# Kernel tuning notes

Hardware: AMD Instinct MI355X
Metric: run time of the kernel (lower is better)

## Reference

```python
import jax, jax.numpy as jnp
import numpy as np

NUM_ITER = 3  # Newton-Schulz iterations (init kwarg)

def setup_inputs() -> dict:
    key = jax.random.key(0)
    x = jax.random.normal(key, (64, 28, 28, 256), dtype=jnp.float32)
    return {"x": x}

def reference(x):
    B, H, W, C = x.shape
    n = H * W
    # Faithful to K.reshape(inputs, (batch, C, n)) -- a plain row-major reshape
    X = x.reshape(B, C, n)
    # Sigma = X @ I_hat @ X^T with I_hat = (1/n)(I - (1/n) 11^T), i.e. the
    # centering projector: identical to mean-centering then (1/n) Xc Xc^T.
    Xc = X - X.mean(axis=2, keepdims=True)            # [B, C, n]
    Sigma = jnp.einsum('bcn,bdn->bcd', Xc, Xc) / n    # [B, C, C]
    trace = jnp.trace(Sigma, axis1=1, axis2=2)[:, None, None]  # [B,1,1]
    A = Sigma / trace
    I = jnp.eye(C, dtype=x.dtype)
    I3 = 3.0 * I
    Y = A
    Z = jnp.broadcast_to(I, (B, C, C))
    # Newton-Schulz: NOTE original updates Z with the already-updated Y
    for _ in range(NUM_ITER):
        Y = 0.5 * jnp.matmul(Y, I3 - jnp.matmul(Z, Y))
        Z = 0.5 * jnp.matmul(I3 - jnp.matmul(Z, Y), Z)
    Cmat = jnp.sqrt(trace) * Y                        # [B, C, C]
    # Upper-triangular (incl. diagonal) vectorization, row-major order
    iu_r, iu_c = jnp.triu_indices(C)
    return Cmat[:, iu_r, iu_c]                        # [B, C*(C+1)/2]
```

## Files before the change

### kernel.cpp

```cpp
#include <hip/hip_runtime.h>
#include <math.h>

#define BATCH 64
#define CD 256
#define NX 784
#define TRIU_N 32896
#define MSZ 65536
#define REG_STRIDE 1032
#define ARR_STRIDE 4128
#define BUF_STRIDE 16512

typedef unsigned short ushort_t;
typedef unsigned int uint_t;
typedef __attribute__((ext_vector_type(8))) short short8;
typedef __attribute__((ext_vector_type(16))) float floatx16;

__device__ __forceinline__ void decode_bid(int bid, int& tile, int& bb) {
    int xcd = bid & 7, g = bid >> 3;
    tile = g & 3;
    bb = ((g >> 2) << 3) | xcd;
}

__device__ __forceinline__ float bf2f(ushort_t h) {
    return __uint_as_float(((uint_t)h) << 16);
}
__device__ __forceinline__ void pack2(float f0, float f1, uint_t& hp, uint_t& lp) {
    uint_t h, l;
    asm("v_cvt_pk_bf16_f32 %0, %1, %2" : "=v"(h) : "v"(f0), "v"(f1));
    float r0 = f0 - __uint_as_float(h << 16);
    float r1 = f1 - __uint_as_float(h & 0xffff0000u);
    asm("v_cvt_pk_bf16_f32 %0, %1, %2" : "=v"(l) : "v"(r0), "v"(r1));
    hp = h; lp = l;
}
__device__ __forceinline__ void store8(ushort_t* H, ushort_t* L, const float* y) {
    uint_t hw[4], lw[4];
    #pragma unroll
    for (int i = 0; i < 4; ++i) pack2(y[2*i], y[2*i+1], hw[i], lw[i]);
    *(uint4*)H = make_uint4(hw[0], hw[1], hw[2], hw[3]);
    *(uint4*)L = make_uint4(lw[0], lw[1], lw[2], lw[3]);
}

__device__ __forceinline__ int swoff(int r, int c) {
    int p = r >> 7, s = (c >> 5) & 7, ks = (c >> 4) & 1, kh = (c >> 3) & 1;
    return ((((p * 8 + s) * 2 + ks) * 2 + kh) * 128 + (r & 127)) * 8 + (c & 7);
}

__device__ __forceinline__ void rawbar() {
    __builtin_amdgcn_s_barrier();
    __builtin_amdgcn_sched_barrier(0);
}

__device__ __forceinline__ void mfma_stage8(const ushort_t* us, int bufbase,
                                            int wr, int wcp, int khalf, int lrow,
                                            floatx16* acc) {
    __builtin_amdgcn_s_setprio(1);
    #pragma unroll
    for (int ks = 0; ks < 2; ++ks) {
        const int rid = ks * 2 + khalf;
        const ushort_t* rb = us + bufbase + rid * REG_STRIDE + lrow * 8;
        short8 aH = *(const short8*)(rb + wr * 256);
        short8 aL = *(const short8*)(rb + ARR_STRIDE + wr * 256);
        #pragma unroll
        for (int cq = 0; cq < 2; ++cq) {
            const int col = wcp * 2 + cq;
            short8 bH = *(const short8*)(rb + 2 * ARR_STRIDE + col * 256);
            short8 bL = *(const short8*)(rb + 3 * ARR_STRIDE + col * 256);
            acc[cq] = __builtin_amdgcn_mfma_f32_32x32x16_bf16(aH, bH, acc[cq], 0, 0, 0);
            acc[cq] = __builtin_amdgcn_mfma_f32_32x32x16_bf16(aH, bL, acc[cq], 0, 0, 0);
            acc[cq] = __builtin_amdgcn_mfma_f32_32x32x16_bf16(aL, bH, acc[cq], 0, 0, 0);
        }
    }
    __builtin_amdgcn_s_setprio(0);
}

__device__ __forceinline__ void acc_bounce(float* fsmem, const floatx16* acc,
                                           int wr, int wcp, int khalf, int lrow) {
    __syncthreads();
    #pragma unroll
    for (int cq = 0; cq < 2; ++cq)
        #pragma unroll
        for (int i = 0; i < 16; ++i) {
            int rl = (i & 3) + ((i >> 2) << 3) + (khalf << 2);
            fsmem[(wr * 32 + rl) * 129 + (wcp * 2 + cq) * 32 + lrow] = acc[cq][i];
        }
    __syncthreads();
}

struct Cur { float4 v[2][2]; };

__device__ __forceinline__ void gr_load(const float* Xb, int rowBase, int colBase, int s,
                                        const int* side, const int* srow, const int* skq,
                                        Cur& c) {
    #pragma unroll
    for (int q = 0; q < 2; ++q) {
        int gk = s * 32 + skq[q] * 8;
        if (gk < NX) {
            const float* p = Xb + (size_t)((side[q] ? colBase : rowBase) + srow[q]) * NX + gk;
            c.v[q][0] = *(const float4*)p;
            c.v[q][1] = *(const float4*)(p + 4);
        } else {
            c.v[q][0] = make_float4(0.f, 0.f, 0.f, 0.f);
            c.v[q][1] = make_float4(0.f, 0.f, 0.f, 0.f);
        }
    }
}

__device__ __forceinline__ void gr_conv(ushort_t* us, int bufbase, const Cur& c,
                                        const int* side, const int* srow, const int* skq,
                                        float* rs) {
    #pragma unroll
    for (int q = 0; q < 2; ++q) {
        float f[8] = {c.v[q][0].x, c.v[q][0].y, c.v[q][0].z, c.v[q][0].w,
                      c.v[q][1].x, c.v[q][1].y, c.v[q][1].z, c.v[q][1].w};
        rs[q] += ((f[0] + f[1]) + (f[2] + f[3])) + ((f[4] + f[5]) + (f[6] + f[7]));
        uint_t hp[4], lp[4];
        #pragma unroll
        for (int i = 0; i < 4; ++i) pack2(f[2*i], f[2*i+1], hp[i], lp[i]);
        int base = bufbase + (side[q] * 2) * ARR_STRIDE + skq[q] * REG_STRIDE + srow[q] * 8;
        *(uint4*)(us + base)              = make_uint4(hp[0], hp[1], hp[2], hp[3]);
        *(uint4*)(us + base + ARR_STRIDE) = make_uint4(lp[0], lp[1], lp[2], lp[3]);
    }
}

__global__ __launch_bounds__(512, 1)
void gram_mfma(const float* __restrict__ X, float* __restrict__ means,
               float* __restrict__ tr,
               ushort_t* __restrict__ Gh, ushort_t* __restrict__ Gl) {
    __shared__ __align__(16) float fsmem[16512];
    __shared__ float dsh[8];
    ushort_t* us = (ushort_t*)fsmem;
    int tile, bb;
    decode_bid(blockIdx.x, tile, bb);
    const int rowBase = (tile >> 1) * 128, colBase = (tile & 1) * 128;
    const int tid = threadIdx.x, lane = tid & 63, wv = tid >> 6;
    const int wr = wv >> 1, wcp = wv & 1;
    const int khalf = lane >> 5, lrow = lane & 31;
    const float* Xb = X + (size_t)bb * CD * NX;

    floatx16 acc[2];
    #pragma unroll
    for (int cq = 0; cq < 2; ++cq)
        #pragma unroll
        for (int i = 0; i < 16; ++i) acc[cq][i] = 0.f;

    int side[2], srow[2], skq[2];
    #pragma unroll
    for (int q = 0; q < 2; ++q) {
        int gid = q * 512 + tid;
        side[q] = gid >> 9;
        srow[q] = (gid >> 2) & 127;
        skq[q]  = gid & 3;
    }
    float rs[2] = {0.f, 0.f};

    Cur curA, curB;
    gr_load(Xb, rowBase, colBase, 0, side, srow, skq, curA);
    gr_load(Xb, rowBase, colBase, 1, side, srow, skq, curB);
    gr_conv(us, 0, curA, side, srow, skq, rs);

    for (int s = 0; s < 25; s += 2) {
        asm volatile("s_waitcnt lgkmcnt(0)" ::: "memory");
        rawbar();
        if (s + 2 <= 24) gr_load(Xb, rowBase, colBase, s + 2, side, srow, skq, curA);
        mfma_stage8(us, 0, wr, wcp, khalf, lrow, acc);
        if (s + 1 <= 24) gr_conv(us, BUF_STRIDE, curB, side, srow, skq, rs);
        if (s + 1 <= 24) {
            asm volatile("s_waitcnt lgkmcnt(0)" ::: "memory");
            rawbar();
            if (s + 3 <= 24) gr_load(Xb, rowBase, colBase, s + 3, side, srow, skq, curB);
            mfma_stage8(us, BUF_STRIDE, wr, wcp, khalf, lrow, acc);
            gr_conv(us, 0, curA, side, srow, skq, rs);
        }
    }

    {
        float r0 = rs[0], r1 = rs[1];
        r0 += __shfl_xor(r0, 1, 64); r0 += __shfl_xor(r0, 2, 64);
        r1 += __shfl_xor(r1, 1, 64); r1 += __shfl_xor(r1, 2, 64);
        if ((tid & 3) == 0) {
            int rr = tid >> 2;
            means[bb * CD + rowBase + rr] = r0 * (1.0f / NX);
            means[bb * CD + colBase + rr] = r1 * (1.0f / NX);
        }
    }

    acc_bounce(fsmem, acc, wr, wcp, khalf, lrow);
    const int rloc = tid & 127;
    const int r = rowBase + rloc;
    const float mr = means[bb * CD + r];
    const bool diagblk = (rowBase == colBase);
    float dv = 0.f;
    #pragma unroll
    for (int gi = 0; gi < 4; ++gi) {
        int g = (tid >> 7) + gi * 4;
        int c0 = colBase + g * 8;
        int so = swoff(r, c0);
        float v[8];
        #pragma unroll
        for (int j = 0; j < 8; ++j) {
            v[j] = fsmem[rloc * 129 + g * 8 + j] * (1.0f / NX) - mr * means[bb * CD + c0 + j];
            if (diagblk && (c0 + j) == r) dv += v[j];
        }
        store8(Gh + (size_t)bb * MSZ + so, Gl + (size_t)bb * MSZ + so, v);
    }
    if (diagblk) {
        for (int off = 32; off; off >>= 1) dv += __shfl_down(dv, off, 64);
        if (lane == 0) dsh[wv] = dv;
        __syncthreads();
        if (tid == 0) {
            float s = ((dsh[0] + dsh[1]) + (dsh[2] + dsh[3]))
                    + ((dsh[4] + dsh[5]) + (dsh[6] + dsh[7]));
            atomicAdd(&tr[bb], s);
        }
    }
}

__device__ __forceinline__ void ns_prefetch(const ushort_t* const* arrp, ushort_t* us,
                                            int wv, int lane, int s, int buf) {
    #pragma unroll
    for (int j = 0; j < 4; ++j) {
        int ck = wv * 4 + j;
        int arr = ck >> 3, rid = (ck >> 1) & 3, half = ck & 1;
        const ushort_t* g = arrp[arr] + s * 4096 + rid * 1024 + half * 512 + lane * 8;
        ushort_t* l = us + buf * BUF_STRIDE + arr * ARR_STRIDE + rid * REG_STRIDE + half * 512;
        __builtin_amdgcn_global_load_lds(
            (const __attribute__((address_space(1))) unsigned int*)g,
            (__attribute__((address_space(3))) unsigned int*)l, 16, 0, 0);
    }
}

template<int MODE>
__global__ __launch_bounds__(512, 1)
void ns_mfma(const ushort_t* __restrict__ Ah, const ushort_t* __restrict__ Al,
             const ushort_t* __restrict__ Bh, const ushort_t* __restrict__ Bl,
             const ushort_t* __restrict__ Mh, const ushort_t* __restrict__ Ml,
             const float* __restrict__ tr,
             ushort_t* __restrict__ O1h, ushort_t* __restrict__ O1l,
             ushort_t* __restrict__ O2h, ushort_t* __restrict__ O2l,
             float* __restrict__ outT) {
    int tile, bb;
    decode_bid(blockIdx.x, tile, bb);
    const int rowBase = (tile >> 1) * 128, colBase = (tile & 1) * 128;
    if (MODE == 3 && rowBase > colBase) return;
    __shared__ __align__(16) float fsmem[33024];
    ushort_t* us = (ushort_t*)fsmem;
    const size_t mb = (size_t)bb * MSZ;
    const int tid = threadIdx.x, lane = tid & 63, wv = tid >> 6;
    const int wr = wv >> 1, wcp = wv & 1;
    const int khalf = lane >> 5, lrow = lane & 31;
    const ushort_t* arrp[4] = {
        Ah + mb + (size_t)(rowBase >> 7) * 32768,
        Al + mb + (size_t)(rowBase >> 7) * 32768,
        Bh + mb + (size_t)(colBase >> 7) * 32768,
        Bl + mb + (size_t)(colBase >> 7) * 32768 };

    floatx16 acc[2];
    #pragma unroll
    for (int cq = 0; cq < 2; ++cq)
        #pragma unroll
        for (int i = 0; i < 16; ++i) acc[cq][i] = 0.f;

    ns_prefetch(arrp, us, wv, lane, 0, 0);
    ns_prefetch(arrp, us, wv, lane, 1, 1);
    ns_prefetch(arrp, us, wv, lane, 2, 2);
    #pragma unroll
    for (int s = 0; s < 8; ++s) {
        if (s <= 5)      asm volatile("s_waitcnt vmcnt(8)" ::: "memory");
        else if (s == 6) asm volatile("s_waitcnt vmcnt(4)" ::: "memory");
        else             asm volatile("s_waitcnt vmcnt(0)" ::: "memory");
        rawbar();
        mfma_stage8(us, (s & 3) * BUF_STRIDE, wr, wcp, khalf, lrow, acc);
        if (s < 5) ns_prefetch(arrp, us, wv, lane, s + 3, (s + 3) & 3);
    }

    acc_bounce(fsmem, acc, wr, wcp, khalf, lrow);
    const int rloc = tid & 127;
    const int r = rowBase + rloc;
    float it = 0.f, st = 0.f;
    if (MODE == 2) it = 1.0f / tr[bb];
    if (MODE == 3) st = sqrtf(tr[bb]);
    #pragma unroll
    for (int gi = 0; gi < 4; ++gi) {
        int g = (tid >> 7) + gi * 4;
        int c0 = colBase + g * 8;
        int so = swoff(r, c0);
        float v[8];
        #pragma unroll
        for (int j = 0; j < 8; ++j) v[j] = fsmem[rloc * 129 + g * 8 + j];
        if (MODE == 0) {
            store8(O1h + mb + so, O1l + mb + so, v);
        } else {
            float mv[8];
            {
                const ushort_t* mhp = Mh + mb + so;
                const ushort_t* mlp = Ml + mb + so;
                uint4 mh4 = *(const uint4*)mhp;
                uint4 ml4 = *(const uint4*)mlp;
                const uint_t mhw[4] = {mh4.x, mh4.y, mh4.z, mh4.w};
                const uint_t mlw[4] = {ml4.x, ml4.y, ml4.z, ml4.w};
                #pragma unroll
                for (int i = 0; i < 4; ++i) {
                    mv[2*i]   = __uint_as_float(mhw[i] << 16) + __uint_as_float(mlw[i] << 16);
                    mv[2*i+1] = __uint_as_float(mhw[i] & 0xffff0000u) + __uint_as_float(mlw[i] & 0xffff0000u);
                }
            }
            if (MODE == 1) {
                float y[8];
                #pragma unroll
                for (int j = 0; j < 8; ++j) y[j] = fmaf(1.5f, mv[j], -0.5f * v[j]);
                store8(O1h + mb + so, O1l + mb + so, y);
            } else if (MODE == 2) {
                float y[8], z[8];
                #pragma unroll
                for (int j = 0; j < 8; ++j) {
                    y[j] = 1.5f * it * mv[j] - 0.5f * it * it * v[j];
                    z[j] = ((r == c0 + j) ? 1.5f : 0.f) - 0.5f * y[j];
                }
                store8(O1h + mb + so, O1l + mb + so, y);
                store8(O2h + mb + so, O2l + mb + so, z);
            } else if (MODE == 4) {
                float w[8];
                #pragma unroll
                for (int j = 0; j < 8; ++j)
                    w[j] = ((r == c0 + j) ? 2.25f : 0.f) - 1.5f * mv[j] + 0.25f * v[j];
                store8(O1h + mb + so, O1l + mb + so, v);
                store8(O2h + mb + so, O2l + mb + so, w);
            } else {
                int tb = r * CD - (r * (r - 1)) / 2 - r;
                #pragma unroll
                for (int j = 0; j < 8; ++j) {
                    float y = fmaf(1.5f, mv[j], -0.5f * v[j]);
                    int c = c0 + j;
                    if (c >= r) outT[(size_t)bb * TRIU_N + tb + c] = st * y;
                }
            }
        }
    }
}

extern "C" void kernel_launch(void* const* d_in, const int* in_sizes, int n_in,
                              void* d_out, int out_size, void* d_ws, size_t ws_size,
                              hipStream_t stream) {
    const float* x = (const float*)d_in[0];
    float* out = (float*)d_out;
    char* ws = (char*)d_ws;
    const size_t HS = (size_t)BATCH * MSZ * 2;
    ushort_t* S0h = (ushort_t*)(ws + 0 * HS);
    ushort_t* S0l = (ushort_t*)(ws + 1 * HS);
    ushort_t* S1h = (ushort_t*)(ws + 2 * HS);
    ushort_t* S1l = (ushort_t*)(ws + 3 * HS);
    ushort_t* S2h = (ushort_t*)(ws + 4 * HS);
    ushort_t* S2l = (ushort_t*)(ws + 5 * HS);
    ushort_t* S3h = (ushort_t*)(ws + 6 * HS);
    ushort_t* S3l = (ushort_t*)(ws + 7 * HS);
    ushort_t* S4h = (ushort_t*)(ws + 8 * HS);
    ushort_t* S4l = (ushort_t*)(ws + 9 * HS);
    float* means = (float*)(ws + 10 * HS);
    float* tr = means + BATCH * CD;

    hipMemsetAsync(tr, 0, BATCH * sizeof(float), stream);
    gram_mfma<<<256, 512, 0, stream>>>(x, means, tr, S0h, S0l);
    ns_mfma<2><<<256, 512, 0, stream>>>(S0h, S0l, S0h, S0l, S0h, S0l, tr,
                                        S1h, S1l, S2h, S2l, nullptr);
    ns_mfma<4><<<256, 512, 0, stream>>>(S1h, S1l, S1h, S1l, S1h, S1l, tr,
                                        S3h, S3l, S0h, S0l, nullptr);
    ns_mfma<1><<<256, 512, 0, stream>>>(S2h, S2l, S3h, S3l, S1h, S1l, tr,
                                        S4h, S4l, nullptr, nullptr, nullptr);
    ns_mfma<1><<<256, 512, 0, stream>>>(S0h, S0l, S4h, S4l, S2h, S2l, tr,
                                        S1h, S1l, nullptr, nullptr, nullptr);
    ns_mfma<0><<<256, 512, 0, stream>>>(S4h, S4l, S4h, S4l, nullptr, nullptr, tr,
                                        S3h, S3l, nullptr, nullptr, nullptr);
    ns_mfma<3><<<256, 512, 0, stream>>>(S1h, S1l, S3h, S3l, S4h, S4l, tr,
                                        nullptr, nullptr, nullptr, nullptr, out);
}
```

Measured before the change: 203.1 us.

## Split output tiles to 128x64 with 256-thread blocks, two per CU

Each block now computes a 128x64 output tile instead of 128x128, so 512 blocks of 256 threads launch per kernel with launch bounds allowing two blocks per CU. The LDS layout is rebuilt with separate A and B regions sized for the narrower B tile. The NS prefetch pipeline drops from four to three stages to fit the smaller shared-memory budget. The aim is better CU occupancy and load balance with 256 CUs, and finer triangular skipping in the final stage, at the cost of reloading A tiles twice as often and a shallower prefetch depth.

```diff
diff --git a/kernel.cpp b/kernel.cpp
--- a/kernel.cpp
+++ b/kernel.cpp
@@ -7,8 +7,11 @@
 #define TRIU_N 32896
 #define MSZ 65536
 #define REG_STRIDE 1032
-#define ARR_STRIDE 4128
-#define BUF_STRIDE 16512
+#define A_ARR 4128
+#define B_BASE 8256
+#define B_REG 520
+#define B_ARR 2080
+#define STG 12416
 
 typedef unsigned short ushort_t;
 typedef unsigned int uint_t;
@@ -17,8 +20,8 @@
 
 __device__ __forceinline__ void decode_bid(int bid, int& tile, int& bb) {
     int xcd = bid & 7, g = bid >> 3;
-    tile = g & 3;
-    bb = ((g >> 2) << 3) | xcd;
+    tile = g & 7;
+    bb = ((g >> 3) << 3) | xcd;
 }
 
 __device__ __forceinline__ float bf2f(ushort_t h) {
@@ -50,21 +53,21 @@
     __builtin_amdgcn_sched_barrier(0);
 }
 
-__device__ __forceinline__ void mfma_stage8(const ushort_t* us, int bufbase,
-                                            int wr, int wcp, int khalf, int lrow,
+__device__ __forceinline__ void mfma_stage4(const ushort_t* us, int bufbase,
+                                            int wv, int khalf, int lrow,
                                             floatx16* acc) {
     __builtin_amdgcn_s_setprio(1);
     #pragma unroll
     for (int ks = 0; ks < 2; ++ks) {
         const int rid = ks * 2 + khalf;
-        const ushort_t* rb = us + bufbase + rid * REG_STRIDE + lrow * 8;
-        short8 aH = *(const short8*)(rb + wr * 256);
-        short8 aL = *(const short8*)(rb + ARR_STRIDE + wr * 256);
+        const ushort_t* ra = us + bufbase + rid * REG_STRIDE + wv * 256 + lrow * 8;
+        short8 aH = *(const short8*)(ra);
+        short8 aL = *(const short8*)(ra + A_ARR);
+        const ushort_t* rb = us + bufbase + B_BASE + rid * B_REG + lrow * 8;
         #pragma unroll
         for (int cq = 0; cq < 2; ++cq) {
-            const int col = wcp * 2 + cq;
-            short8 bH = *(const short8*)(rb + 2 * ARR_STRIDE + col * 256);
-            short8 bL = *(const short8*)(rb + 3 * ARR_STRIDE + col * 256);
+            short8 bH = *(const short8*)(rb + cq * 256);
+            short8 bL = *(const short8*)(rb + B_ARR + cq * 256);
             acc[cq] = __builtin_amdgcn_mfma_f32_32x32x16_bf16(aH, bH, acc[cq], 0, 0, 0);
             acc[cq] = __builtin_amdgcn_mfma_f32_32x32x16_bf16(aH, bL, acc[cq], 0, 0, 0);
             acc[cq] = __builtin_amdgcn_mfma_f32_32x32x16_bf16(aL, bH, acc[cq], 0, 0, 0);
@@ -74,28 +77,29 @@
 }
 
 __device__ __forceinline__ void acc_bounce(float* fsmem, const floatx16* acc,
-                                           int wr, int wcp, int khalf, int lrow) {
+                                           int wv, int khalf, int lrow) {
     __syncthreads();
     #pragma unroll
     for (int cq = 0; cq < 2; ++cq)
         #pragma unroll
         for (int i = 0; i < 16; ++i) {
             int rl = (i & 3) + ((i >> 2) << 3) + (khalf << 2);
-            fsmem[(wr * 32 + rl) * 129 + (wcp * 2 + cq) * 32 + lrow] = acc[cq][i];
+            fsmem[(wv * 32 + rl) * 65 + cq * 32 + lrow] = acc[cq][i];
         }
     __syncthreads();
 }
 
-struct Cur { float4 v[2][2]; };
+struct Cur { float4 v[3][2]; };
 
 __device__ __forceinline__ void gr_load(const float* Xb, int rowBase, int colBase, int s,
-                                        const int* side, const int* srow, const int* skq,
-                                        Cur& c) {
-    #pragma unroll
-    for (int q = 0; q < 2; ++q) {
-        int gk = s * 32 + skq[q] * 8;
+                                        int tid, Cur& c) {
+    const int kq = tid & 3, rr = tid >> 2;
+    const int xrow[3] = {rowBase + rr, rowBase + 64 + rr, colBase + rr};
+    int gk = s * 32 + kq * 8;
+    #pragma unroll
+    for (int q = 0; q < 3; ++q) {
         if (gk < NX) {
-            const float* p = Xb + (size_t)((side[q] ? colBase : rowBase) + srow[q]) * NX + gk;
+            const float* p = Xb + (size_t)xrow[q] * NX + gk;
             c.v[q][0] = *(const float4*)p;
             c.v[q][1] = *(const float4*)(p + 4);
         } else {
@@ -106,34 +110,37 @@
 }
 
 __device__ __forceinline__ void gr_conv(ushort_t* us, int bufbase, const Cur& c,
-                                        const int* side, const int* srow, const int* skq,
-                                        float* rs) {
-    #pragma unroll
-    for (int q = 0; q < 2; ++q) {
+                                        int tid, float* rs) {
+    const int kq = tid & 3, rr = tid >> 2;
+    const int lbase[3] = {kq * REG_STRIDE + rr * 8,
+                          kq * REG_STRIDE + 512 + rr * 8,
+                          B_BASE + kq * B_REG + rr * 8};
+    const int lostep[3] = {A_ARR, A_ARR, B_ARR};
+    #pragma unroll
+    for (int q = 0; q < 3; ++q) {
         float f[8] = {c.v[q][0].x, c.v[q][0].y, c.v[q][0].z, c.v[q][0].w,
                       c.v[q][1].x, c.v[q][1].y, c.v[q][1].z, c.v[q][1].w};
         rs[q] += ((f[0] + f[1]) + (f[2] + f[3])) + ((f[4] + f[5]) + (f[6] + f[7]));
         uint_t hp[4], lp[4];
         #pragma unroll
         for (int i = 0; i < 4; ++i) pack2(f[2*i], f[2*i+1], hp[i], lp[i]);
-        int base = bufbase + (side[q] * 2) * ARR_STRIDE + skq[q] * REG_STRIDE + srow[q] * 8;
-        *(uint4*)(us + base)              = make_uint4(hp[0], hp[1], hp[2], hp[3]);
-        *(uint4*)(us + base + ARR_STRIDE) = make_uint4(lp[0], lp[1], lp[2], lp[3]);
-    }
-}
-
-__global__ __launch_bounds__(512, 1)
+        int base = bufbase + lbase[q];
+        *(uint4*)(us + base)             = make_uint4(hp[0], hp[1], hp[2], hp[3]);
+        *(uint4*)(us + base + lostep[q]) = make_uint4(lp[0], lp[1], lp[2], lp[3]);
+    }
+}
+
+__global__ __launch_bounds__(256, 2)
 void gram_mfma(const float* __restrict__ X, float* __restrict__ means,
                float* __restrict__ tr,
                ushort_t* __restrict__ Gh, ushort_t* __restrict__ Gl) {
-    __shared__ __align__(16) float fsmem[16512];
-    __shared__ float dsh[8];
+    __shared__ __align__(16) float fsmem[12416];
+    __shared__ float dsh[4];
     ushort_t* us = (ushort_t*)fsmem;
     int tile, bb;
     decode_bid(blockIdx.x, tile, bb);
-    const int rowBase = (tile >> 1) * 128, colBase = (tile & 1) * 128;
+    const int rowBase = (tile >> 2) * 128, colBase = (tile & 3) * 64;
     const int tid = threadIdx.x, lane = tid & 63, wv = tid >> 6;
-    const int wr = wv >> 1, wcp = wv & 1;
     const int khalf = lane >> 5, lrow = lane & 31;
     const float* Xb = X + (size_t)bb * CD * NX;
 
@@ -143,62 +150,55 @@
         #pragma unroll
         for (int i = 0; i < 16; ++i) acc[cq][i] = 0.f;
 
-    int side[2], srow[2], skq[2];
-    #pragma unroll
-    for (int q = 0; q < 2; ++q) {
-        int gid = q * 512 + tid;
-        side[q] = gid >> 9;
-        srow[q] = (gid >> 2) & 127;
-        skq[q]  = gid & 3;
-    }
-    float rs[2] = {0.f, 0.f};
-
+    float rs[3] = {0.f, 0.f, 0.f};
     Cur curA, curB;
-    gr_load(Xb, rowBase, colBase, 0, side, srow, skq, curA);
-    gr_load(Xb, rowBase, colBase, 1, side, srow, skq, curB);
-    gr_conv(us, 0, curA, side, srow, skq, rs);
+    gr_load(Xb, rowBase, colBase, 0, tid, curA);
+    gr_load(Xb, rowBase, colBase, 1, tid, curB);
+    gr_conv(us, 0, curA, tid, rs);
 
     for (int s = 0; s < 25; s += 2) {
         asm volatile("s_waitcnt lgkmcnt(0)" ::: "memory");
         rawbar();
-        if (s + 2 <= 24) gr_load(Xb, rowBase, colBase, s + 2, side, srow, skq, curA);
-        mfma_stage8(us, 0, wr, wcp, khalf, lrow, acc);
-        if (s + 1 <= 24) gr_conv(us, BUF_STRIDE, curB, side, srow, skq, rs);
+        if (s + 2 <= 24) gr_load(Xb, rowBase, colBase, s + 2, tid, curA);
+        mfma_stage4(us, 0, wv, khalf, lrow, acc);
+        if (s + 1 <= 24) gr_conv(us, STG, curB, tid, rs);
         if (s + 1 <= 24) {
             asm volatile("s_waitcnt lgkmcnt(0)" ::: "memory");
             rawbar();
-            if (s + 3 <= 24) gr_load(Xb, rowBase, colBase, s + 3, side, srow, skq, curB);
-            mfma_stage8(us, BUF_STRIDE, wr, wcp, khalf, lrow, acc);
-            gr_conv(us, 0, curA, side, srow, skq, rs);
+            if (s + 3 <= 24) gr_load(Xb, rowBase, colBase, s + 3, tid, curB);
+            mfma_stage4(us, STG, wv, khalf, lrow, acc);
+            gr_conv(us, 0, curA, tid, rs);
         }
     }
 
     {
-        float r0 = rs[0], r1 = rs[1];
+        float r0 = rs[0], r1 = rs[1], r2 = rs[2];
         r0 += __shfl_xor(r0, 1, 64); r0 += __shfl_xor(r0, 2, 64);
         r1 += __shfl_xor(r1, 1, 64); r1 += __shfl_xor(r1, 2, 64);
+        r2 += __shfl_xor(r2, 1, 64); r2 += __shfl_xor(r2, 2, 64);
         if ((tid & 3) == 0) {
             int rr = tid >> 2;
-            means[bb * CD + rowBase + rr] = r0 * (1.0f / NX);
-            means[bb * CD + colBase + rr] = r1 * (1.0f / NX);
-        }
-    }
-
-    acc_bounce(fsmem, acc, wr, wcp, khalf, lrow);
+            means[bb * CD + rowBase + rr]      = r0 * (1.0f / NX);
+            means[bb * CD + rowBase + 64 + rr] = r1 * (1.0f / NX);
+            means[bb * CD + colBase + rr]      = r2 * (1.0f / NX);
+        }
+    }
+
+    acc_bounce(fsmem, acc, wv, khalf, lrow);
     const int rloc = tid & 127;
     const int r = rowBase + rloc;
     const float mr = means[bb * CD + r];
-    const bool diagblk = (rowBase == colBase);
+    const bool diagblk = ((colBase >> 7) == (rowBase >> 7));
     float dv = 0.f;
     #pragma unroll
     for (int gi = 0; gi < 4; ++gi) {
-        int g = (tid >> 7) + gi * 4;
+        int g = (tid >> 7) + gi * 2;
         int c0 = colBase + g * 8;
         int so = swoff(r, c0);
         float v[8];
         #pragma unroll
         for (int j = 0; j < 8; ++j) {
-            v[j] = fsmem[rloc * 129 + g * 8 + j] * (1.0f / NX) - mr * means[bb * CD + c0 + j];
+            v[j] = fsmem[rloc * 65 + g * 8 + j] * (1.0f / NX) - mr * means[bb * CD + c0 + j];
             if (diagblk && (c0 + j) == r) dv += v[j];
         }
         store8(Gh + (size_t)bb * MSZ + so, Gl + (size_t)bb * MSZ + so, v);
@@ -207,22 +207,29 @@
         for (int off = 32; off; off >>= 1) dv += __shfl_down(dv, off, 64);
         if (lane == 0) dsh[wv] = dv;
         __syncthreads();
-        if (tid == 0) {
-            float s = ((dsh[0] + dsh[1]) + (dsh[2] + dsh[3]))
-                    + ((dsh[4] + dsh[5]) + (dsh[6] + dsh[7]));
-            atomicAdd(&tr[bb], s);
-        }
-    }
-}
-
-__device__ __forceinline__ void ns_prefetch(const ushort_t* const* arrp, ushort_t* us,
-                                            int wv, int lane, int s, int buf) {
-    #pragma unroll
-    for (int j = 0; j < 4; ++j) {
-        int ck = wv * 4 + j;
-        int arr = ck >> 3, rid = (ck >> 1) & 3, half = ck & 1;
-        const ushort_t* g = arrp[arr] + s * 4096 + rid * 1024 + half * 512 + lane * 8;
-        ushort_t* l = us + buf * BUF_STRIDE + arr * ARR_STRIDE + rid * REG_STRIDE + half * 512;
+        if (tid == 0)
+            atomicAdd(&tr[bb], (dsh[0] + dsh[1]) + (dsh[2] + dsh[3]));
+    }
+}
+
+__device__ __forceinline__ void ns_prefetch(const ushort_t* const* arrp, int bhalf,
+                                            ushort_t* us, int wv, int lane,
+                                            int s, int buf) {
+    #pragma unroll
+    for (int j = 0; j < 6; ++j) {
+        int ck = wv * 6 + j;
+        const ushort_t* g;
+        ushort_t* l;
+        if (ck < 16) {
+            int arr = ck >> 3, rid = (ck >> 1) & 3, half = ck & 1;
+            g = arrp[arr] + s * 4096 + rid * 1024 + half * 512 + lane * 8;
+            l = us + buf + arr * A_ARR + rid * REG_STRIDE + half * 512;
+        } else {
+            int ck2 = ck - 16;
+            int arr = ck2 >> 2, rid = ck2 & 3;
+            g = arrp[2 + arr] + s * 4096 + rid * 1024 + bhalf * 512 + lane * 8;
+            l = us + buf + B_BASE + arr * B_ARR + rid * B_REG;
+        }
         __builtin_amdgcn_global_load_lds(
             (const __attribute__((address_space(1))) unsigned int*)g,
             (__attribute__((address_space(3))) unsigned int*)l, 16, 0, 0);
@@ -230,7 +237,7 @@
 }
 
 template<int MODE>
-__global__ __launch_bounds__(512, 1)
+__global__ __launch_bounds__(256, 2)
 void ns_mfma(const ushort_t* __restrict__ Ah, const ushort_t* __restrict__ Al,
              const ushort_t* __restrict__ Bh, const ushort_t* __restrict__ Bl,
              const ushort_t* __restrict__ Mh, const ushort_t* __restrict__ Ml,
@@ -240,14 +247,14 @@
              float* __restrict__ outT) {
     int tile, bb;
     decode_bid(blockIdx.x, tile, bb);
-    const int rowBase = (tile >> 1) * 128, colBase = (tile & 1) * 128;
-    if (MODE == 3 && rowBase > colBase) return;
-    __shared__ __align__(16) float fsmem[33024];
+    const int rowBase = (tile >> 2) * 128, colBase = (tile & 3) * 64;
+    if (MODE == 3 && colBase + 64 <= rowBase) return;
+    __shared__ __align__(16) float fsmem[18624];
     ushort_t* us = (ushort_t*)fsmem;
     const size_t mb = (size_t)bb * MSZ;
     const int tid = threadIdx.x, lane = tid & 63, wv = tid >> 6;
-    const int wr = wv >> 1, wcp = wv & 1;
     const int khalf = lane >> 5, lrow = lane & 31;
+    const int bhalf = (colBase >> 6) & 1;
     const ushort_t* arrp[4] = {
         Ah + mb + (size_t)(rowBase >> 7) * 32768,
         Al + mb + (size_t)(rowBase >> 7) * 32768,
@@ -260,20 +267,18 @@
         #pragma unroll
         for (int i = 0; i < 16; ++i) acc[cq][i] = 0.f;
 
-    ns_prefetch(arrp, us, wv, lane, 0, 0);
-    ns_prefetch(arrp, us, wv, lane, 1, 1);
-    ns_prefetch(arrp, us, wv, lane, 2, 2);
+    ns_prefetch(arrp, bhalf, us, wv, lane, 0, 0);
+    ns_prefetch(arrp, bhalf, us, wv, lane, 1, STG);
     #pragma unroll
     for (int s = 0; s < 8; ++s) {
-        if (s <= 5)      asm volatile("s_waitcnt vmcnt(8)" ::: "memory");
-        else if (s == 6) asm volatile("s_waitcnt vmcnt(4)" ::: "memory");
-        else             asm volatile("s_waitcnt vmcnt(0)" ::: "memory");
+        if (s < 7) asm volatile("s_waitcnt vmcnt(6)" ::: "memory");
+        else       asm volatile("s_waitcnt vmcnt(0)" ::: "memory");
         rawbar();
-        mfma_stage8(us, (s & 3) * BUF_STRIDE, wr, wcp, khalf, lrow, acc);
-        if (s < 5) ns_prefetch(arrp, us, wv, lane, s + 3, (s + 3) & 3);
-    }
-
-    acc_bounce(fsmem, acc, wr, wcp, khalf, lrow);
+        if (s < 6) ns_prefetch(arrp, bhalf, us, wv, lane, s + 2, ((s + 2) % 3) * STG);
+        mfma_stage4(us, (s % 3) * STG, wv, khalf, lrow, acc);
+    }
+
+    acc_bounce(fsmem, acc, wv, khalf, lrow);
     const int rloc = tid & 127;
     const int r = rowBase + rloc;
     float it = 0.f, st = 0.f;
@@ -281,21 +286,19 @@
     if (MODE == 3) st = sqrtf(tr[bb]);
     #pragma unroll
     for (int gi = 0; gi < 4; ++gi) {
-        int g = (tid >> 7) + gi * 4;
+        int g = (tid >> 7) + gi * 2;
         int c0 = colBase + g * 8;
         int so = swoff(r, c0);
         float v[8];
         #pragma unroll
-        for (int j = 0; j < 8; ++j) v[j] = fsmem[rloc * 129 + g * 8 + j];
+        for (int j = 0; j < 8; ++j) v[j] = fsmem[rloc * 65 + g * 8 + j];
         if (MODE == 0) {
             store8(O1h + mb + so, O1l + mb + so, v);
         } else {
             float mv[8];
             {
-                const ushort_t* mhp = Mh + mb + so;
-                const ushort_t* mlp = Ml + mb + so;
-                uint4 mh4 = *(const uint4*)mhp;
-                uint4 ml4 = *(const uint4*)mlp;
+                uint4 mh4 = *(const uint4*)(Mh + mb + so);
+                uint4 ml4 = *(const uint4*)(Ml + mb + so);
                 const uint_t mhw[4] = {mh4.x, mh4.y, mh4.z, mh4.w};
                 const uint_t mlw[4] = {ml4.x, ml4.y, ml4.z, ml4.w};
                 #pragma unroll
@@ -359,17 +362,17 @@
     float* tr = means + BATCH * CD;
 
     hipMemsetAsync(tr, 0, BATCH * sizeof(float), stream);
-    gram_mfma<<<256, 512, 0, stream>>>(x, means, tr, S0h, S0l);
-    ns_mfma<2><<<256, 512, 0, stream>>>(S0h, S0l, S0h, S0l, S0h, S0l, tr,
+    gram_mfma<<<512, 256, 0, stream>>>(x, means, tr, S0h, S0l);
+    ns_mfma<2><<<512, 256, 0, stream>>>(S0h, S0l, S0h, S0l, S0h, S0l, tr,
                                         S1h, S1l, S2h, S2l, nullptr);
-    ns_mfma<4><<<256, 512, 0, stream>>>(S1h, S1l, S1h, S1l, S1h, S1l, tr,
+    ns_mfma<4><<<512, 256, 0, stream>>>(S1h, S1l, S1h, S1l, S1h, S1l, tr,
                                         S3h, S3l, S0h, S0l, nullptr);
-    ns_mfma<1><<<256, 512, 0, stream>>>(S2h, S2l, S3h, S3l, S1h, S1l, tr,
+    ns_mfma<1><<<512, 256, 0, stream>>>(S2h, S2l, S3h, S3l, S1h, S1l, tr,
                                         S4h, S4l, nullptr, nullptr, nullptr);
-    ns_mfma<1><<<256, 512, 0, stream>>>(S0h, S0l, S4h, S4l, S2h, S2l, tr,
+    ns_mfma<1><<<512, 256, 0, stream>>>(S0h, S0l, S4h, S4l, S2h, S2l, tr,
                                         S1h, S1l, nullptr, nullptr, nullptr);
-    ns_mfma<0><<<256, 512, 0, stream>>>(S4h, S4l, S4h, S4l, nullptr, nullptr, tr,
+    ns_mfma<0><<<512, 256, 0, stream>>>(S4h, S4l, S4h, S4l, nullptr, nullptr, tr,
                                         S3h, S3l, nullptr, nullptr, nullptr);
-    ns_mfma<3><<<256, 512, 0, stream>>>(S1h, S1l, S3h, S3l, S4h, S4l, tr,
+    ns_mfma<3><<<512, 256, 0, stream>>>(S1h, S1l, S3h, S3l, S4h, S4l, tr,
                                         nullptr, nullptr, nullptr, nullptr, out);
 }
```

New measurement: 219.6 us. 8.1% more time.

## Fuse gram and Newton-Schulz kernels into one persistent kernel with per-batch barriers

Applied to the files above, without the earlier changes.

Replaces the seven separate launches with a single persistent kernel. The four tile blocks of each batch element synchronize through atomic counters in global memory between phases, instead of relying on kernel boundaries. This removes launch overhead and device-wide drains between dependent stages, and lets different batches progress independently. The cost is spin-wait barriers, which depend on all 256 blocks being co-resident. It also merges two independent NS phases with no barrier between them and moves the trace reciprocal and sqrt to a single load.

```diff
diff --git a/kernel.cpp b/kernel.cpp
--- a/kernel.cpp
+++ b/kernel.cpp
@@ -47,6 +47,18 @@
 
 __device__ __forceinline__ void rawbar() {
     __builtin_amdgcn_s_barrier();
+    __builtin_amdgcn_sched_barrier(0);
+}
+
+__device__ __forceinline__ void gbar(unsigned* bars, int slot) {
+    __syncthreads();
+    if (threadIdx.x == 0) {
+        __hip_atomic_fetch_add(&bars[slot], 1u, __ATOMIC_RELEASE, __HIP_MEMORY_SCOPE_AGENT);
+        while (__hip_atomic_load(&bars[slot], __ATOMIC_RELAXED, __HIP_MEMORY_SCOPE_AGENT) < 4u)
+            __builtin_amdgcn_s_sleep(4);
+        __builtin_amdgcn_fence(__ATOMIC_ACQUIRE, "agent");
+    }
+    __syncthreads();
     __builtin_amdgcn_sched_barrier(0);
 }
 
@@ -122,15 +134,12 @@
     }
 }
 
-__global__ __launch_bounds__(512, 1)
-void gram_mfma(const float* __restrict__ X, float* __restrict__ means,
-               float* __restrict__ tr,
-               ushort_t* __restrict__ Gh, ushort_t* __restrict__ Gl) {
-    __shared__ __align__(16) float fsmem[16512];
-    __shared__ float dsh[8];
+__device__ __forceinline__ void gram_phase(float* fsmem, const float* __restrict__ X,
+                                           float* __restrict__ means, float* __restrict__ tr,
+                                           ushort_t* __restrict__ Gh, ushort_t* __restrict__ Gl,
+                                           int tile, int bb) {
     ushort_t* us = (ushort_t*)fsmem;
-    int tile, bb;
-    decode_bid(blockIdx.x, tile, bb);
+    float* dsh = fsmem + 16512;
     const int rowBase = (tile >> 1) * 128, colBase = (tile & 1) * 128;
     const int tid = threadIdx.x, lane = tid & 63, wv = tid >> 6;
     const int wr = wv >> 1, wcp = wv & 1;
@@ -230,19 +239,17 @@
 }
 
 template<int MODE>
-__global__ __launch_bounds__(512, 1)
-void ns_mfma(const ushort_t* __restrict__ Ah, const ushort_t* __restrict__ Al,
-             const ushort_t* __restrict__ Bh, const ushort_t* __restrict__ Bl,
-             const ushort_t* __restrict__ Mh, const ushort_t* __restrict__ Ml,
-             const float* __restrict__ tr,
-             ushort_t* __restrict__ O1h, ushort_t* __restrict__ O1l,
-             ushort_t* __restrict__ O2h, ushort_t* __restrict__ O2l,
-             float* __restrict__ outT) {
-    int tile, bb;
-    decode_bid(blockIdx.x, tile, bb);
+__device__ __forceinline__ void ns_phase(float* fsmem, int tile, int bb,
+    const ushort_t* __restrict__ Ah, const ushort_t* __restrict__ Al,
+    const ushort_t* __restrict__ Bh, const ushort_t* __restrict__ Bl,
+    const ushort_t* __restrict__ Mh, const ushort_t* __restrict__ Ml,
+    float it, float st,
+    ushort_t* __restrict__ O1h, ushort_t* __restrict__ O1l,
+    ushort_t* __restrict__ O2h, ushort_t* __restrict__ O2l,
+    float* __restrict__ outT) {
     const int rowBase = (tile >> 1) * 128, colBase = (tile & 1) * 128;
     if (MODE == 3 && rowBase > colBase) return;
-    __shared__ __align__(16) float fsmem[33024];
+    __syncthreads();
     ushort_t* us = (ushort_t*)fsmem;
     const size_t mb = (size_t)bb * MSZ;
     const int tid = threadIdx.x, lane = tid & 63, wv = tid >> 6;
@@ -276,9 +283,6 @@
     acc_bounce(fsmem, acc, wr, wcp, khalf, lrow);
     const int rloc = tid & 127;
     const int r = rowBase + rloc;
-    float it = 0.f, st = 0.f;
-    if (MODE == 2) it = 1.0f / tr[bb];
-    if (MODE == 3) st = sqrtf(tr[bb]);
     #pragma unroll
     for (int gi = 0; gi < 4; ++gi) {
         int g = (tid >> 7) + gi * 4;
@@ -292,10 +296,8 @@
         } else {
             float mv[8];
             {
-                const ushort_t* mhp = Mh + mb + so;
-                const ushort_t* mlp = Ml + mb + so;
-                uint4 mh4 = *(const uint4*)mhp;
-                uint4 ml4 = *(const uint4*)mlp;
+                uint4 mh4 = *(const uint4*)(Mh + mb + so);
+                uint4 ml4 = *(const uint4*)(Ml + mb + so);
                 const uint_t mhw[4] = {mh4.x, mh4.y, mh4.z, mh4.w};
                 const uint_t mlw[4] = {ml4.x, ml4.y, ml4.z, ml4.w};
                 #pragma unroll
@@ -338,6 +340,43 @@
     }
 }
 
+__global__ __launch_bounds__(512, 1)
+void fused_all(const float* __restrict__ X,
+               ushort_t* __restrict__ S0h, ushort_t* __restrict__ S0l,
+               ushort_t* __restrict__ S1h, ushort_t* __restrict__ S1l,
+               ushort_t* __restrict__ S2h, ushort_t* __restrict__ S2l,
+               ushort_t* __restrict__ S3h, ushort_t* __restrict__ S3l,
+               ushort_t* __restrict__ S4h, ushort_t* __restrict__ S4l,
+               float* __restrict__ means, float* __restrict__ tr,
+               float* __restrict__ outT, unsigned* __restrict__ bars) {
+    __shared__ __align__(16) float fsmem[33024];
+    int tile, bb;
+    decode_bid(blockIdx.x, tile, bb);
+
+    gram_phase(fsmem, X, means, tr, S0h, S0l, tile, bb);
+    gbar(bars, bb * 8 + 0);
+
+    const float trv = tr[bb];
+    const float it = 1.0f / trv, st = sqrtf(trv);
+
+    ns_phase<2>(fsmem, tile, bb, S0h, S0l, S0h, S0l, S0h, S0l, it, 0.f,
+                S1h, S1l, S2h, S2l, nullptr);
+    gbar(bars, bb * 8 + 1);
+    ns_phase<4>(fsmem, tile, bb, S1h, S1l, S1h, S1l, S1h, S1l, 0.f, 0.f,
+                S3h, S3l, S0h, S0l, nullptr);
+    gbar(bars, bb * 8 + 2);
+    ns_phase<1>(fsmem, tile, bb, S2h, S2l, S3h, S3l, S1h, S1l, 0.f, 0.f,
+                S4h, S4l, nullptr, nullptr, nullptr);
+    gbar(bars, bb * 8 + 3);
+    ns_phase<1>(fsmem, tile, bb, S0h, S0l, S4h, S4l, S2h, S2l, 0.f, 0.f,
+                S1h, S1l, nullptr, nullptr, nullptr);
+    ns_phase<0>(fsmem, tile, bb, S4h, S4l, S4h, S4l, nullptr, nullptr, 0.f, 0.f,
+                S3h, S3l, nullptr, nullptr, nullptr);
+    gbar(bars, bb * 8 + 4);
+    ns_phase<3>(fsmem, tile, bb, S1h, S1l, S3h, S3l, S4h, S4l, 0.f, st,
+                nullptr, nullptr, nullptr, nullptr, outT);
+}
+
 extern "C" void kernel_launch(void* const* d_in, const int* in_sizes, int n_in,
                               void* d_out, int out_size, void* d_ws, size_t ws_size,
                               hipStream_t stream) {
@@ -357,19 +396,9 @@
     ushort_t* S4l = (ushort_t*)(ws + 9 * HS);
     float* means = (float*)(ws + 10 * HS);
     float* tr = means + BATCH * CD;
-
-    hipMemsetAsync(tr, 0, BATCH * sizeof(float), stream);
-    gram_mfma<<<256, 512, 0, stream>>>(x, means, tr, S0h, S0l);
-    ns_mfma<2><<<256, 512, 0, stream>>>(S0h, S0l, S0h, S0l, S0h, S0l, tr,
-                                        S1h, S1l, S2h, S2l, nullptr);
-    ns_mfma<4><<<256, 512, 0, stream>>>(S1h, S1l, S1h, S1l, S1h, S1l, tr,
-                                        S3h, S3l, S0h, S0l, nullptr);
-    ns_mfma<1><<<256, 512, 0, stream>>>(S2h, S2l, S3h, S3l, S1h, S1l, tr,
-                                        S4h, S4l, nullptr, nullptr, nullptr);
-    ns_mfma<1><<<256, 512, 0, stream>>>(S0h, S0l, S4h, S4l, S2h, S2l, tr,
-                                        S1h, S1l, nullptr, nullptr, nullptr);
-    ns_mfma<0><<<256, 512, 0, stream>>>(S4h, S4l, S4h, S4l, nullptr, nullptr, tr,
-                                        S3h, S3l, nullptr, nullptr, nullptr);
-    ns_mfma<3><<<256, 512, 0, stream>>>(S1h, S1l, S3h, S3l, S4h, S4l, tr,
-                                        nullptr, nullptr, nullptr, nullptr, out);
-}
+    unsigned* bars = (unsigned*)(tr + BATCH);
+
+    hipMemsetAsync(tr, 0, BATCH * sizeof(float) + BATCH * 8 * sizeof(unsigned), stream);
+    fused_all<<<256, 512, 0, stream>>>(x, S0h, S0l, S1h, S1l, S2h, S2l,
+                                       S3h, S3l, S4h, S4l, means, tr, out, bars);
+}
```

Measured after the change: 220.3 us. 8.4% more time.
